# Kernel optimization log

Hardware: AMD Instinct MI355X
Metric: run time of the kernel (lower is better)

## Reference

```python
import jax, jax.numpy as jnp
import numpy as np

N_NODES = 100000
N_EDGES = 1600000
IN_SIZE = 128
HIDDEN = 32
OUT_SIZE = 16


def _mean_agg(h, src, dst, n_nodes):
    # segment-sum of source features into destination nodes, then divide by in-degree
    summed = jax.ops.segment_sum(h[src], dst, num_segments=n_nodes)  # [N, D]
    deg = jax.ops.segment_sum(jnp.ones((src.shape[0],), h.dtype), dst, num_segments=n_nodes)
    return summed / jnp.maximum(deg, 1.0)[:, None]


def _sage_layer(h, src, dst, W_self, W_neigh, b):
    # DGL SAGEConv (mean): fc_self(h) + fc_neigh(mean_neigh(h)) + bias
    agg = _mean_agg(h, src, dst, h.shape[0])
    return h @ W_self + agg @ W_neigh + b


def setup_inputs() -> dict:
    key = jax.random.key(0)
    ks = jax.random.split(key, 9)
    inp = {
        "x": jax.random.normal(ks[0], (N_NODES, IN_SIZE), jnp.float32),
        "edge_src": jax.random.randint(ks[1], (N_EDGES,), 0, N_NODES, jnp.int32),
        "edge_dst": jax.random.randint(ks[2], (N_EDGES,), 0, N_NODES, jnp.int32),
        "W_self1": jax.random.normal(ks[3], (IN_SIZE, HIDDEN), jnp.float32) / np.sqrt(IN_SIZE),
        "W_neigh1": jax.random.normal(ks[4], (IN_SIZE, HIDDEN), jnp.float32) / np.sqrt(IN_SIZE),
        "b1": jnp.zeros((HIDDEN,), jnp.float32),
        "W_self2": jax.random.normal(ks[5], (HIDDEN, HIDDEN), jnp.float32) / np.sqrt(HIDDEN),
        "W_neigh2": jax.random.normal(ks[6], (HIDDEN, HIDDEN), jnp.float32) / np.sqrt(HIDDEN),
        "b2": jnp.zeros((HIDDEN,), jnp.float32),
        "W_self3": jax.random.normal(ks[7], (HIDDEN, OUT_SIZE), jnp.float32) / np.sqrt(HIDDEN),
        "W_neigh3": jax.random.normal(ks[8], (HIDDEN, OUT_SIZE), jnp.float32) / np.sqrt(HIDDEN),
        "b3": jnp.zeros((OUT_SIZE,), jnp.float32),
    }
    return inp


def reference(x, edge_src, edge_dst,
              W_self1, W_neigh1, b1,
              W_self2, W_neigh2, b2,
              W_self3, W_neigh3, b3):
    h = jax.nn.relu(_sage_layer(x, edge_src, edge_dst, W_self1, W_neigh1, b1))
    h = jax.nn.relu(_sage_layer(h, edge_src, edge_dst, W_self2, W_neigh2, b2))
    h = _sage_layer(h, edge_src, edge_dst, W_self3, W_neigh3, b3)
    return h
```

## Files before the change

### kernel.cpp

```cpp
#include <hip/hip_runtime.h>


#define BLOCK 256
#define NBLK 256
#define BSH 9
#define CAP 12288

__global__ void hist_kernel(const int* __restrict__ dst, int* __restrict__ hist,
                            int n_edges, int nbuk, int ch) {
    __shared__ int cnt[256];
    int tid = threadIdx.x;
    for (int i = tid; i < nbuk; i += BLOCK) cnt[i] = 0;
    __syncthreads();
    int e0 = blockIdx.x * ch;
    int e1 = e0 + ch; if (e1 > n_edges) e1 = n_edges;
    for (int e = e0 + tid; e < e1; e += BLOCK)
        atomicAdd(&cnt[dst[e] >> BSH], 1);
    __syncthreads();
    for (int i = tid; i < nbuk; i += BLOCK)
        hist[i * NBLK + blockIdx.x] = cnt[i];
}

__global__ void scanBlk_kernel(int* __restrict__ hist, int* __restrict__ buktot) {
    int b = blockIdx.x;
    int tid = threadIdx.x;
    int orig = hist[b * NBLK + tid];
    int v = orig;
    int lane = tid & 63, w = tid >> 6;
#pragma unroll
    for (int off = 1; off < 64; off <<= 1) {
        int u = __shfl_up(v, off);
        if (lane >= off) v += u;
    }
    __shared__ int wps[4];
    if (lane == 63) wps[w] = v;
    __syncthreads();
    int wadd = 0;
    for (int k = 0; k < w; ++k) wadd += wps[k];
    int excl = v - orig + wadd;
    hist[b * NBLK + tid] = excl;
    if (tid == 255) buktot[b] = excl + orig;
}

__global__ void scanBuk_kernel(const int* __restrict__ buktot, int* __restrict__ bukoff,
                               int nbuk, int* __restrict__ startp, int n_nodes, int n_edges) {
    int tid = threadIdx.x;
    int orig = (tid < nbuk) ? buktot[tid] : 0;
    int v = orig;
    int lane = tid & 63, w = tid >> 6;
#pragma unroll
    for (int off = 1; off < 64; off <<= 1) {
        int u = __shfl_up(v, off);
        if (lane >= off) v += u;
    }
    __shared__ int wps[4];
    if (lane == 63) wps[w] = v;
    __syncthreads();
    int wadd = 0;
    for (int k = 0; k < w; ++k) wadd += wps[k];
    int excl = v - orig + wadd;
    if (tid < nbuk) bukoff[tid] = excl;
    if (tid == 0) { bukoff[nbuk] = n_edges; startp[n_nodes] = n_edges; }
}

__global__ void part_kernel(const int* __restrict__ src, const int* __restrict__ dst,
                            const int* __restrict__ hist, const int* __restrict__ bukoff,
                            unsigned* __restrict__ pairs, int n_edges, int nbuk, int ch) {
    __shared__ int base[256];
    __shared__ int cnt[256];
    int tid = threadIdx.x;
    for (int i = tid; i < nbuk; i += BLOCK) {
        base[i] = hist[i * NBLK + blockIdx.x] + bukoff[i];
        cnt[i] = 0;
    }
    __syncthreads();
    int e0 = blockIdx.x * ch;
    int e1 = e0 + ch; if (e1 > n_edges) e1 = n_edges;
    for (int e = e0 + tid; e < e1; e += BLOCK) {
        int d = dst[e];
        int b = d >> BSH;
        unsigned dl = (unsigned)(d & ((1 << BSH) - 1));
        int r = atomicAdd(&cnt[b], 1);
        pairs[base[b] + r] = (unsigned)src[e] | (dl << 20);
    }
}

__global__ void build_kernel(const unsigned* __restrict__ pairs, const int* __restrict__ bukoff,
                             int* __restrict__ start, float* __restrict__ invdeg,
                             int* __restrict__ csr_src, int n_nodes) {
    __shared__ int deg[512];
    __shared__ int lst[512];
    __shared__ int cur[512];
    __shared__ int wps[4];
    __shared__ int scsr[CAP];

    int b = blockIdx.x;
    int tid = threadIdx.x;
    int e0 = bukoff[b];
    int e1 = bukoff[b + 1];
    int lo = b << BSH;
    int hi = lo + (1 << BSH); if (hi > n_nodes) hi = n_nodes;
    int nn = hi - lo;
    int ne = e1 - e0;

    for (int i = tid; i < 512; i += BLOCK) deg[i] = 0;
    __syncthreads();
    for (int i = e0 + tid; i < e1; i += BLOCK)
        atomicAdd(&deg[pairs[i] >> 20], 1);
    __syncthreads();

    int d0 = deg[2 * tid], d1 = deg[2 * tid + 1];
    int s = d0 + d1;
    int lane = tid & 63, w = tid >> 6;
    int v = s;
#pragma unroll
    for (int off = 1; off < 64; off <<= 1) {
        int u = __shfl_up(v, off);
        if (lane >= off) v += u;
    }
    if (lane == 63) wps[w] = v;
    __syncthreads();
    int wb = 0;
    for (int k = 0; k < w; ++k) wb += wps[k];
    int excl = wb + v - s;
    lst[2 * tid] = excl;
    lst[2 * tid + 1] = excl + d0;
    cur[2 * tid] = 0;
    cur[2 * tid + 1] = 0;
    __syncthreads();

    for (int i = tid; i < nn; i += BLOCK) {
        start[lo + i] = e0 + lst[i];
        int d = deg[i];
        invdeg[lo + i] = 1.0f / (float)(d < 1 ? 1 : d);
    }

    if (ne <= CAP) {
        for (int i = e0 + tid; i < e1; i += BLOCK) {
            unsigned pr = pairs[i];
            int dl = pr >> 20;
            int sl = lst[dl] + atomicAdd(&cur[dl], 1);
            scsr[sl] = (int)(pr & 0xFFFFFu);
        }
        __syncthreads();
        for (int i = tid; i < ne; i += BLOCK) csr_src[e0 + i] = scsr[i];
    } else {
        for (int i = e0 + tid; i < e1; i += BLOCK) {
            unsigned pr = pairs[i];
            int dl = pr >> 20;
            int sl = lst[dl] + atomicAdd(&cur[dl], 1);
            csr_src[e0 + sl] = (int)(pr & 0xFFFFFu);
        }
    }
}

template<int DIN, int DOUT, int OPT, int NPT>
__global__ __launch_bounds__(256, 4)
void proj_reg(const float* __restrict__ h,
              const float* __restrict__ Ws,
              const float* __restrict__ Wn,
              const float* __restrict__ bias,
              float* __restrict__ pre,
              float* __restrict__ p,
              int n_nodes) {
    constexpr int OD  = 2 * DOUT;
    constexpr int OG  = OD / OPT;
    constexpr int NG  = 256 / OG;
    constexpr int NT  = NPT * NG;
    constexpr int NV  = OPT / 4;

    __shared__ float sW[DIN][OD];
    __shared__ float sb[DOUT];

    const int tid = threadIdx.x;
    for (int i = tid; i < DIN * OD; i += 256) {
        int k = i / OD, o = i % OD;
        sW[k][o] = (o < DOUT) ? Ws[k * DOUT + o] : Wn[k * DOUT + (o - DOUT)];
    }
    if (tid < DOUT) sb[tid] = bias[tid];
    __syncthreads();

    const int to = tid % OG;
    const int tn = tid / OG;
    const int o0 = to * OPT;
    const int node0 = blockIdx.x * NT + tn * NPT;

    const float4* __restrict__ xp[NPT];
#pragma unroll
    for (int n = 0; n < NPT; ++n) {
        int node = node0 + n;
        int safe = (node < n_nodes) ? node : (n_nodes - 1);
        xp[n] = reinterpret_cast<const float4*>(h + (size_t)safe * DIN);
    }

    float acc[NPT][OPT];
#pragma unroll
    for (int n = 0; n < NPT; ++n)
#pragma unroll
        for (int o = 0; o < OPT; ++o) acc[n][o] = 0.f;

#pragma unroll 2
    for (int k4 = 0; k4 < DIN / 4; ++k4) {
        float4 xv[NPT];
#pragma unroll
        for (int n = 0; n < NPT; ++n) xv[n] = xp[n][k4];
#pragma unroll
        for (int kk = 0; kk < 4; kk += 2) {
            int k = 4 * k4 + kk;
            float4 w0[NV], w1[NV];
#pragma unroll
            for (int v = 0; v < NV; ++v) {
                w0[v] = *reinterpret_cast<const float4*>(&sW[k][o0 + 4 * v]);
                w1[v] = *reinterpret_cast<const float4*>(&sW[k + 1][o0 + 4 * v]);
            }
#pragma unroll
            for (int n = 0; n < NPT; ++n) {
                float xk = reinterpret_cast<const float*>(&xv[n])[kk];
#pragma unroll
                for (int v = 0; v < NV; ++v) {
                    acc[n][4 * v + 0] = fmaf(xk, w0[v].x, acc[n][4 * v + 0]);
                    acc[n][4 * v + 1] = fmaf(xk, w0[v].y, acc[n][4 * v + 1]);
                    acc[n][4 * v + 2] = fmaf(xk, w0[v].z, acc[n][4 * v + 2]);
                    acc[n][4 * v + 3] = fmaf(xk, w0[v].w, acc[n][4 * v + 3]);
                }
            }
#pragma unroll
            for (int n = 0; n < NPT; ++n) {
                float xk = reinterpret_cast<const float*>(&xv[n])[kk + 1];
#pragma unroll
                for (int v = 0; v < NV; ++v) {
                    acc[n][4 * v + 0] = fmaf(xk, w1[v].x, acc[n][4 * v + 0]);
                    acc[n][4 * v + 1] = fmaf(xk, w1[v].y, acc[n][4 * v + 1]);
                    acc[n][4 * v + 2] = fmaf(xk, w1[v].z, acc[n][4 * v + 2]);
                    acc[n][4 * v + 3] = fmaf(xk, w1[v].w, acc[n][4 * v + 3]);
                }
            }
        }
    }

    const bool self_half = (o0 < DOUT);
    const int oo = self_half ? o0 : (o0 - DOUT);
    float* __restrict__ dstbuf = self_half ? pre : p;
#pragma unroll
    for (int n = 0; n < NPT; ++n) {
        int node = node0 + n;
        if (node >= n_nodes) continue;
#pragma unroll
        for (int v = 0; v < NV; ++v) {
            float4 r;
            r.x = acc[n][4 * v + 0];
            r.y = acc[n][4 * v + 1];
            r.z = acc[n][4 * v + 2];
            r.w = acc[n][4 * v + 3];
            if (self_half) {
                r.x += sb[oo + 4 * v + 0];
                r.y += sb[oo + 4 * v + 1];
                r.z += sb[oo + 4 * v + 2];
                r.w += sb[oo + 4 * v + 3];
            }
            *reinterpret_cast<float4*>(dstbuf + (size_t)node * DOUT + oo + 4 * v) = r;
        }
    }
}

template<int D, bool RELU>
__global__ void gather_kernel(const float* __restrict__ p,
                              const int* __restrict__ csr_src,
                              const int* __restrict__ start,
                              const float* __restrict__ pre,
                              const float* __restrict__ invdeg,
                              float* __restrict__ out,
                              int n_nodes) {
    constexpr int NPW = 64 / D;
    int wave = threadIdx.x >> 6;
    int lane = threadIdx.x & 63;
    int g = (blockIdx.x * (blockDim.x >> 6) + wave) * NPW + lane / D;
    int f = lane % D;
    if (g >= n_nodes) return;
    int s0 = start[g];
    int s1 = start[g + 1];
    float a0 = 0.f, a1 = 0.f, a2 = 0.f, a3 = 0.f;
    float a4 = 0.f, a5 = 0.f, a6 = 0.f, a7 = 0.f;
    int j = s0;
    for (; j + 8 <= s1; j += 8) {
        int c0 = csr_src[j + 0], c1 = csr_src[j + 1];
        int c2 = csr_src[j + 2], c3 = csr_src[j + 3];
        int c4 = csr_src[j + 4], c5 = csr_src[j + 5];
        int c6 = csr_src[j + 6], c7 = csr_src[j + 7];
        a0 += p[(size_t)c0 * D + f];
        a1 += p[(size_t)c1 * D + f];
        a2 += p[(size_t)c2 * D + f];
        a3 += p[(size_t)c3 * D + f];
        a4 += p[(size_t)c4 * D + f];
        a5 += p[(size_t)c5 * D + f];
        a6 += p[(size_t)c6 * D + f];
        a7 += p[(size_t)c7 * D + f];
    }
    for (; j + 2 <= s1; j += 2) {
        int c0 = csr_src[j], c1 = csr_src[j + 1];
        a0 += p[(size_t)c0 * D + f];
        a1 += p[(size_t)c1 * D + f];
    }
    if (j < s1) a2 += p[(size_t)csr_src[j] * D + f];
    float a = ((a0 + a1) + (a2 + a3)) + ((a4 + a5) + (a6 + a7));
    size_t o = (size_t)g * D + f;
    float v = pre[o] + a * invdeg[g];
    if (RELU) v = fmaxf(v, 0.f);
    out[o] = v;
}

extern "C" void kernel_launch(void* const* d_in, const int* in_sizes, int n_in,
                              void* d_out, int out_size, void* d_ws, size_t ws_size,
                              hipStream_t stream) {
    const float* x        = (const float*)d_in[0];
    const int*   edge_src = (const int*)d_in[1];
    const int*   edge_dst = (const int*)d_in[2];
    const float* Ws1 = (const float*)d_in[3];
    const float* Wn1 = (const float*)d_in[4];
    const float* b1  = (const float*)d_in[5];
    const float* Ws2 = (const float*)d_in[6];
    const float* Wn2 = (const float*)d_in[7];
    const float* b2  = (const float*)d_in[8];
    const float* Ws3 = (const float*)d_in[9];
    const float* Wn3 = (const float*)d_in[10];
    const float* b3  = (const float*)d_in[11];
    float* out = (float*)d_out;

    const int IN = 128, HID = 32;
    const int n_nodes = in_sizes[0] / IN;
    const int n_edges = in_sizes[1];
    const int nbuk = (n_nodes + (1 << BSH) - 1) >> BSH;
    const int ch   = (n_edges + NBLK - 1) / NBLK;

    char* wsb = (char*)d_ws;
    size_t off = 0;
    auto alloc = [&](size_t bytes) { char* r = wsb + off; off = (off + bytes + 255) & ~(size_t)255; return r; };
    int*   startp = (int*)alloc(((size_t)n_nodes + 1) * sizeof(int));
    float* invdeg = (float*)alloc((size_t)n_nodes * sizeof(float));
    int*   csr    = (int*)alloc((size_t)n_edges * sizeof(int));
    int*   hist   = (int*)alloc((size_t)nbuk * NBLK * sizeof(int));
    int*   buktot = (int*)alloc(256 * sizeof(int));
    int*   bukoff = (int*)alloc(257 * sizeof(int));
    float* B0     = (float*)alloc((size_t)n_nodes * HID * sizeof(float));
    float* B1     = (float*)alloc((size_t)n_nodes * HID * sizeof(float));
    float* B3     = (float*)alloc((size_t)n_nodes * HID * sizeof(float));
    unsigned* pairs = (unsigned*)B0;

    const int gP     = (n_nodes + 63) / 64;
    const int gGat32 = (n_nodes + 7) / 8;
    const int gGat16 = (n_nodes + 15) / 16;

    hist_kernel   <<<NBLK, BLOCK, 0, stream>>>(edge_dst, hist, n_edges, nbuk, ch);
    scanBlk_kernel<<<nbuk, BLOCK, 0, stream>>>(hist, buktot);
    scanBuk_kernel<<<1, BLOCK, 0, stream>>>(buktot, bukoff, nbuk, startp, n_nodes, n_edges);
    part_kernel   <<<NBLK, BLOCK, 0, stream>>>(edge_src, edge_dst, hist, bukoff, pairs, n_edges, nbuk, ch);
    build_kernel  <<<nbuk, BLOCK, 0, stream>>>(pairs, bukoff, startp, invdeg, csr, n_nodes);

    proj_reg<128, 32, 8, 2><<<gP, BLOCK, 0, stream>>>(x, Ws1, Wn1, b1, B0, B1, n_nodes);
    gather_kernel<32, true><<<gGat32, BLOCK, 0, stream>>>(B1, csr, startp, B0, invdeg, B3, n_nodes);

    proj_reg<32, 32, 8, 2><<<gP, BLOCK, 0, stream>>>(B3, Ws2, Wn2, b2, B0, B1, n_nodes);
    gather_kernel<32, true><<<gGat32, BLOCK, 0, stream>>>(B1, csr, startp, B0, invdeg, B3, n_nodes);

    proj_reg<32, 16, 4, 2><<<gP, BLOCK, 0, stream>>>(B3, Ws3, Wn3, b3, B0, B1, n_nodes);
    gather_kernel<16, false><<<gGat16, BLOCK, 0, stream>>>(B1, csr, startp, B0, invdeg, out, n_nodes);
}
```

Before: 205.0 us.

## Split projection into self/neighbor halves over grid.y with register prefetch

The fused self+neighbor projection kernel becomes a kernel launched with a 2-wide grid.y. Each half loads only its own weight matrix into shared memory, which halves LDS use and allows higher occupancy (launch bounds 8 instead of 4). The input rows for the next k-step are now prefetched in registers. In exchange, every node's input row is read twice, once by each half, which doubles input traffic for the DIN=128 first layer. Layer 3 also switches to 8 outputs per thread.

```diff
diff --git a/kernel.cpp b/kernel.cpp
--- a/kernel.cpp
+++ b/kernel.cpp
@@ -155,29 +155,31 @@
 }
 
 template<int DIN, int DOUT, int OPT, int NPT>
-__global__ __launch_bounds__(256, 4)
-void proj_reg(const float* __restrict__ h,
-              const float* __restrict__ Ws,
-              const float* __restrict__ Wn,
-              const float* __restrict__ bias,
-              float* __restrict__ pre,
-              float* __restrict__ p,
-              int n_nodes) {
-    constexpr int OD  = 2 * DOUT;
-    constexpr int OG  = OD / OPT;
+__global__ __launch_bounds__(256, 8)
+void proj_half(const float* __restrict__ h,
+               const float* __restrict__ Ws,
+               const float* __restrict__ Wn,
+               const float* __restrict__ bias,
+               float* __restrict__ pre,
+               float* __restrict__ p,
+               int n_nodes) {
+    constexpr int OG  = DOUT / OPT;
     constexpr int NG  = 256 / OG;
     constexpr int NT  = NPT * NG;
     constexpr int NV  = OPT / 4;
-
-    __shared__ float sW[DIN][OD];
+    constexpr int K4  = DIN / 4;
+
+    __shared__ float sW[DIN * DOUT];
     __shared__ float sb[DOUT];
 
+    const bool self_half = (blockIdx.y == 0);
+    const float* __restrict__ W = self_half ? Ws : Wn;
+
     const int tid = threadIdx.x;
-    for (int i = tid; i < DIN * OD; i += 256) {
-        int k = i / OD, o = i % OD;
-        sW[k][o] = (o < DOUT) ? Ws[k * DOUT + o] : Wn[k * DOUT + (o - DOUT)];
-    }
-    if (tid < DOUT) sb[tid] = bias[tid];
+    for (int i = tid; i < DIN * DOUT / 4; i += 256)
+        *reinterpret_cast<float4*>(&sW[i * 4]) =
+            *reinterpret_cast<const float4*>(W + (size_t)i * 4);
+    if (tid < DOUT) sb[tid] = self_half ? bias[tid] : 0.f;
     __syncthreads();
 
     const int to = tid % OG;
@@ -199,47 +201,39 @@
 #pragma unroll
         for (int o = 0; o < OPT; ++o) acc[n][o] = 0.f;
 
-#pragma unroll 2
-    for (int k4 = 0; k4 < DIN / 4; ++k4) {
-        float4 xv[NPT];
-#pragma unroll
-        for (int n = 0; n < NPT; ++n) xv[n] = xp[n][k4];
-#pragma unroll
-        for (int kk = 0; kk < 4; kk += 2) {
+    float4 xc[NPT];
+#pragma unroll
+    for (int n = 0; n < NPT; ++n) xc[n] = xp[n][0];
+
+    for (int k4 = 0; k4 < K4; ++k4) {
+        float4 xn[NPT];
+        int nk4 = (k4 + 1 < K4) ? (k4 + 1) : k4;
+#pragma unroll
+        for (int n = 0; n < NPT; ++n) xn[n] = xp[n][nk4];
+
+#pragma unroll
+        for (int kk = 0; kk < 4; ++kk) {
             int k = 4 * k4 + kk;
-            float4 w0[NV], w1[NV];
-#pragma unroll
-            for (int v = 0; v < NV; ++v) {
-                w0[v] = *reinterpret_cast<const float4*>(&sW[k][o0 + 4 * v]);
-                w1[v] = *reinterpret_cast<const float4*>(&sW[k + 1][o0 + 4 * v]);
-            }
+            float4 w[NV];
+#pragma unroll
+            for (int v = 0; v < NV; ++v)
+                w[v] = *reinterpret_cast<const float4*>(&sW[k * DOUT + o0 + 4 * v]);
 #pragma unroll
             for (int n = 0; n < NPT; ++n) {
-                float xk = reinterpret_cast<const float*>(&xv[n])[kk];
+                float xk = reinterpret_cast<const float*>(&xc[n])[kk];
 #pragma unroll
                 for (int v = 0; v < NV; ++v) {
-                    acc[n][4 * v + 0] = fmaf(xk, w0[v].x, acc[n][4 * v + 0]);
-                    acc[n][4 * v + 1] = fmaf(xk, w0[v].y, acc[n][4 * v + 1]);
-                    acc[n][4 * v + 2] = fmaf(xk, w0[v].z, acc[n][4 * v + 2]);
-                    acc[n][4 * v + 3] = fmaf(xk, w0[v].w, acc[n][4 * v + 3]);
-                }
-            }
-#pragma unroll
-            for (int n = 0; n < NPT; ++n) {
-                float xk = reinterpret_cast<const float*>(&xv[n])[kk + 1];
-#pragma unroll
-                for (int v = 0; v < NV; ++v) {
-                    acc[n][4 * v + 0] = fmaf(xk, w1[v].x, acc[n][4 * v + 0]);
-                    acc[n][4 * v + 1] = fmaf(xk, w1[v].y, acc[n][4 * v + 1]);
-                    acc[n][4 * v + 2] = fmaf(xk, w1[v].z, acc[n][4 * v + 2]);
-                    acc[n][4 * v + 3] = fmaf(xk, w1[v].w, acc[n][4 * v + 3]);
+                    acc[n][4 * v + 0] = fmaf(xk, w[v].x, acc[n][4 * v + 0]);
+                    acc[n][4 * v + 1] = fmaf(xk, w[v].y, acc[n][4 * v + 1]);
+                    acc[n][4 * v + 2] = fmaf(xk, w[v].z, acc[n][4 * v + 2]);
+                    acc[n][4 * v + 3] = fmaf(xk, w[v].w, acc[n][4 * v + 3]);
                 }
             }
         }
-    }
-
-    const bool self_half = (o0 < DOUT);
-    const int oo = self_half ? o0 : (o0 - DOUT);
+#pragma unroll
+        for (int n = 0; n < NPT; ++n) xc[n] = xn[n];
+    }
+
     float* __restrict__ dstbuf = self_half ? pre : p;
 #pragma unroll
     for (int n = 0; n < NPT; ++n) {
@@ -248,17 +242,11 @@
 #pragma unroll
         for (int v = 0; v < NV; ++v) {
             float4 r;
-            r.x = acc[n][4 * v + 0];
-            r.y = acc[n][4 * v + 1];
-            r.z = acc[n][4 * v + 2];
-            r.w = acc[n][4 * v + 3];
-            if (self_half) {
-                r.x += sb[oo + 4 * v + 0];
-                r.y += sb[oo + 4 * v + 1];
-                r.z += sb[oo + 4 * v + 2];
-                r.w += sb[oo + 4 * v + 3];
-            }
-            *reinterpret_cast<float4*>(dstbuf + (size_t)node * DOUT + oo + 4 * v) = r;
+            r.x = acc[n][4 * v + 0] + sb[o0 + 4 * v + 0];
+            r.y = acc[n][4 * v + 1] + sb[o0 + 4 * v + 1];
+            r.z = acc[n][4 * v + 2] + sb[o0 + 4 * v + 2];
+            r.w = acc[n][4 * v + 3] + sb[o0 + 4 * v + 3];
+            *reinterpret_cast<float4*>(dstbuf + (size_t)node * DOUT + o0 + 4 * v) = r;
         }
     }
 }
@@ -346,7 +334,8 @@
     float* B3     = (float*)alloc((size_t)n_nodes * HID * sizeof(float));
     unsigned* pairs = (unsigned*)B0;
 
-    const int gP     = (n_nodes + 63) / 64;
+    const int gP12   = (n_nodes + 127) / 128;
+    const int gP3    = (n_nodes + 255) / 256;
     const int gGat32 = (n_nodes + 7) / 8;
     const int gGat16 = (n_nodes + 15) / 16;
 
@@ -356,12 +345,12 @@
     part_kernel   <<<NBLK, BLOCK, 0, stream>>>(edge_src, edge_dst, hist, bukoff, pairs, n_edges, nbuk, ch);
     build_kernel  <<<nbuk, BLOCK, 0, stream>>>(pairs, bukoff, startp, invdeg, csr, n_nodes);
 
-    proj_reg<128, 32, 8, 2><<<gP, BLOCK, 0, stream>>>(x, Ws1, Wn1, b1, B0, B1, n_nodes);
+    proj_half<128, 32, 8, 2><<<dim3(gP12, 2), BLOCK, 0, stream>>>(x, Ws1, Wn1, b1, B0, B1, n_nodes);
     gather_kernel<32, true><<<gGat32, BLOCK, 0, stream>>>(B1, csr, startp, B0, invdeg, B3, n_nodes);
 
-    proj_reg<32, 32, 8, 2><<<gP, BLOCK, 0, stream>>>(B3, Ws2, Wn2, b2, B0, B1, n_nodes);
+    proj_half<32, 32, 8, 2><<<dim3(gP12, 2), BLOCK, 0, stream>>>(B3, Ws2, Wn2, b2, B0, B1, n_nodes);
     gather_kernel<32, true><<<gGat32, BLOCK, 0, stream>>>(B1, csr, startp, B0, invdeg, B3, n_nodes);
 
-    proj_reg<32, 16, 4, 2><<<gP, BLOCK, 0, stream>>>(B3, Ws3, Wn3, b3, B0, B1, n_nodes);
+    proj_half<32, 16, 8, 2><<<dim3(gP3, 2), BLOCK, 0, stream>>>(B3, Ws3, Wn3, b3, B0, B1, n_nodes);
     gather_kernel<16, false><<<gGat16, BLOCK, 0, stream>>>(B1, csr, startp, B0, invdeg, out, n_nodes);
 }
```

Result: slower. 754.4 us (+268.0%).
